# Kernel optimization log

Hardware: AMD Instinct MI355X
Metric: run time of the kernel (lower is better)

Reference implementation:

```python
import jax, jax.numpy as jnp
import numpy as np

N = 262144
D = 512
B = 1024  # number of segments/graphs (batch.max()+1 in the torch code)


def setup_inputs() -> dict:
    key = jax.random.key(0)
    k1, k2, k3, k4 = jax.random.split(key, 4)
    x = jax.random.normal(k1, (N, D), dtype=jnp.float32)
    batch = jnp.sort(jax.random.randint(k2, (N,), 0, B, dtype=jnp.int64))
    # score MLP params: Linear(D, D//4) -> Tanh -> Linear(D//4, 1)
    W1 = jax.random.normal(k3, (D, D // 4), dtype=jnp.float32) * (1.0 / np.sqrt(D))
    b1 = jnp.zeros((D // 4,), dtype=jnp.float32)
    W2 = jax.random.normal(k4, (D // 4, 1), dtype=jnp.float32) * (1.0 / np.sqrt(D // 4))
    b2 = jnp.zeros((1,), dtype=jnp.float32)
    return {"x": x, "batch": batch, "W1": W1, "b1": b1, "W2": W2, "b2": b2}


def reference(x, batch, W1, b1, W2, b2):
    # score MLP (dropout inactive at inference)
    scores = jnp.tanh(x @ W1 + b1) @ W2 + b2              # [N, 1]
    scores = scores - jnp.max(scores)                      # global max-shift for stability
    exp_s = jnp.exp(scores)                                # [N, 1]
    denom = jax.ops.segment_sum(exp_s, batch, num_segments=B)  # [B, 1]
    weight = exp_s / (denom[batch] + 1e-8)                 # [N, 1] segment softmax
    out = jax.ops.segment_sum(weight * x, batch, num_segments=B)  # [B, D]
    return out
```

## Files before the change

kernel.cpp:

```cpp
#include <hip/hip_runtime.h>
#include <hip/hip_bf16.h>

typedef _Float16 half8 __attribute__((ext_vector_type(8)));
typedef _Float16 half4v __attribute__((ext_vector_type(4)));
typedef float f32x4 __attribute__((ext_vector_type(4)));

#define BM 128
#define BK 64
#define LDK (BK + 8)

__global__ void prep_w1t(const float* __restrict__ W1, _Float16* __restrict__ W1T) {
    int idx = blockIdx.x * 256 + threadIdx.x;
    int n = idx >> 9;
    int k = idx & 511;
    W1T[idx] = (_Float16)W1[k * 128 + n];
}

__global__ __launch_bounds__(256) void score_kernel(
        const float* __restrict__ x, const _Float16* __restrict__ W1T,
        const float* __restrict__ b1, const float* __restrict__ W2,
        const float* __restrict__ b2, float* __restrict__ scores) {
    __shared__ _Float16 As[BM][LDK];
    __shared__ _Float16 Bs[128][LDK];
    const int tid = threadIdx.x;
    const int wave = tid >> 6, lane = tid & 63;
    const int quad = lane >> 4, col = lane & 15;
    const long row0 = (long)blockIdx.x * BM;

    f32x4 acc[2][8] = {};

    for (int kc = 0; kc < 512; kc += BK) {
        #pragma unroll
        for (int it = 0; it < 8; ++it) {
            int idx = it * 256 + tid;
            int r = idx >> 4, c4 = idx & 15;
            float4 v = *(const float4*)&x[(row0 + r) * 512 + kc + c4 * 4];
            half4v h; h[0] = (_Float16)v.x; h[1] = (_Float16)v.y;
                      h[2] = (_Float16)v.z; h[3] = (_Float16)v.w;
            *(half4v*)&As[r][c4 * 4] = h;
        }
        #pragma unroll
        for (int it = 0; it < 4; ++it) {
            int idx = it * 256 + tid;
            int n = idx >> 3, c8 = idx & 7;
            *(half8*)&Bs[n][c8 * 8] = *(const half8*)&W1T[n * 512 + kc + c8 * 8];
        }
        __syncthreads();
        #pragma unroll
        for (int ks = 0; ks < BK; ks += 32) {
            half8 a[2], bf[8];
            #pragma unroll
            for (int mt = 0; mt < 2; ++mt)
                a[mt] = *(half8*)&As[wave * 32 + mt * 16 + col][ks + quad * 8];
            #pragma unroll
            for (int nt = 0; nt < 8; ++nt)
                bf[nt] = *(half8*)&Bs[nt * 16 + col][ks + quad * 8];
            #pragma unroll
            for (int mt = 0; mt < 2; ++mt)
                #pragma unroll
                for (int nt = 0; nt < 8; ++nt)
                    acc[mt][nt] = __builtin_amdgcn_mfma_f32_16x16x32_f16(
                        a[mt], bf[nt], acc[mt][nt], 0, 0, 0);
        }
        __syncthreads();
    }

    float b1v[8], w2v[8];
    #pragma unroll
    for (int nt = 0; nt < 8; ++nt) {
        b1v[nt] = b1[nt * 16 + col];
        w2v[nt] = W2[nt * 16 + col];
    }
    float bias2 = b2[0];
    #pragma unroll
    for (int mt = 0; mt < 2; ++mt) {
        #pragma unroll
        for (int r = 0; r < 4; ++r) {
            float p = 0.f;
            #pragma unroll
            for (int nt = 0; nt < 8; ++nt)
                p += tanhf(acc[mt][nt][r] + b1v[nt]) * w2v[nt];
            #pragma unroll
            for (int off = 1; off < 16; off <<= 1) p += __shfl_xor(p, off);
            if (col == 0)
                scores[row0 + wave * 32 + mt * 16 + quad * 4 + r] = p + bias2;
        }
    }
}

__global__ void max_part(const float* __restrict__ scores, float* __restrict__ partial, int n) {
    __shared__ float red[256];
    int tid = threadIdx.x;
    float m = -1e30f;
    for (long i = (long)blockIdx.x * 256 + tid; i < n; i += (long)gridDim.x * 256)
        m = fmaxf(m, scores[i]);
    red[tid] = m; __syncthreads();
    for (int s = 128; s > 0; s >>= 1) {
        if (tid < s) red[tid] = fmaxf(red[tid], red[tid + s]);
        __syncthreads();
    }
    if (tid == 0) partial[blockIdx.x] = red[0];
}

__global__ void finalize_max(const float* __restrict__ partial, float* __restrict__ gmax,
                             float* __restrict__ denom, int nseg) {
    __shared__ float red[256];
    int tid = threadIdx.x;
    red[tid] = partial[tid]; __syncthreads();
    for (int s = 128; s > 0; s >>= 1) {
        if (tid < s) red[tid] = fmaxf(red[tid], red[tid + s]);
        __syncthreads();
    }
    if (tid == 0) gmax[0] = red[0];
    for (int b = tid; b < nseg; b += 256) denom[b] = 0.f;
}

__global__ void exp_denom(float* __restrict__ scores, const int* __restrict__ batch,
                          const float* __restrict__ gmax, float* __restrict__ denom, int n) {
    const int lane = threadIdx.x & 63;
    const float gm = gmax[0];
    for (long i = (long)blockIdx.x * blockDim.x + threadIdx.x; i < n;
         i += (long)gridDim.x * blockDim.x) {
        int seg = batch[i];
        float e = __expf(scores[i] - gm);
        scores[i] = e;
        float v = e;
        #pragma unroll
        for (int off = 1; off < 64; off <<= 1) {
            float ov = __shfl_down(v, off);
            int   os = __shfl_down(seg, off);
            if (lane + off < 64 && os == seg) v += ov;
        }
        int pseg = __shfl_up(seg, 1);
        if (lane == 0 || pseg != seg) atomicAdd(&denom[seg], v);
    }
}

__global__ void seg_starts(const int* __restrict__ batch, int* __restrict__ starts,
                           int n, int nseg) {
    for (long i = (long)blockIdx.x * blockDim.x + threadIdx.x; i < n;
         i += (long)gridDim.x * blockDim.x) {
        int s = batch[i];
        int p = (i == 0) ? -1 : batch[i - 1];
        for (int b = p + 1; b <= s; ++b) starts[b] = (int)i;
        if (i == n - 1)
            for (int b = s + 1; b <= nseg; ++b) starts[b] = n;
    }
}

__global__ __launch_bounds__(256) void pool_kernel(
        const float* __restrict__ x, const float* __restrict__ exps,
        const float* __restrict__ denom, const int* __restrict__ starts,
        float* __restrict__ out) {
    __shared__ f32x4 red[128];
    const int b = blockIdx.x;
    const int s0 = starts[b], s1 = starts[b + 1];
    const float dinv = 1.f / (denom[b] + 1e-8f);
    const int team = threadIdx.x >> 7;
    const int tl   = threadIdx.x & 127;
    const int c = tl * 4;
    f32x4 acc = {0.f, 0.f, 0.f, 0.f};
    #pragma unroll 4
    for (int i = s0 + team; i < s1; i += 2) {
        float w = exps[i] * dinv;
        f32x4 xv = *(const f32x4*)&x[(long)i * 512 + c];
        acc += w * xv;
    }
    if (team) red[tl] = acc;
    __syncthreads();
    if (!team) {
        f32x4 o = red[tl];
        acc += o;
        *(f32x4*)&out[(long)b * 512 + c] = acc;
    }
}

extern "C" void kernel_launch(void* const* d_in, const int* in_sizes, int n_in,
                              void* d_out, int out_size, void* d_ws, size_t ws_size,
                              hipStream_t stream) {
    const float* x     = (const float*)d_in[0];
    const int*   batch = (const int*)d_in[1];
    const float* W1    = (const float*)d_in[2];
    const float* b1    = (const float*)d_in[3];
    const float* W2    = (const float*)d_in[4];
    const float* b2    = (const float*)d_in[5];
    float* out = (float*)d_out;

    const int N = in_sizes[1];
    const int D = 512;
    const int NSEG = out_size / D;

    _Float16* W1T   = (_Float16*)d_ws;
    float* scores   = (float*)((char*)d_ws + 131072);
    float* partial  = scores + N;
    float* gmax     = partial + 256;
    float* denom    = partial + 512;
    int*   starts   = (int*)(denom + NSEG);

    prep_w1t<<<256, 256, 0, stream>>>(W1, W1T);
    seg_starts<<<256, 256, 0, stream>>>(batch, starts, N, NSEG);
    score_kernel<<<N / BM, 256, 0, stream>>>(x, W1T, b1, W2, b2, scores);
    max_part<<<256, 256, 0, stream>>>(scores, partial, N);
    finalize_max<<<1, 256, 0, stream>>>(partial, gmax, denom, NSEG);
    exp_denom<<<256, 256, 0, stream>>>(scores, batch, gmax, denom, N);
    pool_kernel<<<NSEG, 256, 0, stream>>>(x, scores, denom, starts, out);
}
```

Before: 807.6 us.

## Fuse score MLP, exp and segment pooling into one kernel with atomics

Merges the score GEMM, exponentiation and weighted segment pooling into a single kernel. Each 128-row tile exponentiates its scores in shared memory, then re-reads its own x rows (likely still in cache) and atomically accumulates per-segment sums and denominators. A final pass divides by the denominator. This removes the second full pass over x from HBM, the stored scores array and several small kernels. In exchange it drops the global max shift, which risks overflow for large scores, adds many float atomics, and hardcodes the output and segment sizes.

```diff
diff --git a/kernel.cpp b/kernel.cpp
--- a/kernel.cpp
+++ b/kernel.cpp
@@ -1,5 +1,4 @@
 #include <hip/hip_runtime.h>
-#include <hip/hip_bf16.h>
 
 typedef _Float16 half8 __attribute__((ext_vector_type(8)));
 typedef _Float16 half4v __attribute__((ext_vector_type(4)));
@@ -16,16 +15,28 @@
     W1T[idx] = (_Float16)W1[k * 128 + n];
 }
 
-__global__ __launch_bounds__(256) void score_kernel(
+__global__ void zero_kernel(float* __restrict__ out, float* __restrict__ denom) {
+    int id = blockIdx.x * 256 + threadIdx.x;
+    f32x4 z = {0.f, 0.f, 0.f, 0.f};
+    if (id < 131072)           ((f32x4*)out)[id] = z;
+    else                       ((f32x4*)denom)[id - 131072] = z;
+}
+
+__global__ __launch_bounds__(256) void fused_kernel(
         const float* __restrict__ x, const _Float16* __restrict__ W1T,
         const float* __restrict__ b1, const float* __restrict__ W2,
-        const float* __restrict__ b2, float* __restrict__ scores) {
+        const float* __restrict__ b2, const int* __restrict__ batch,
+        float* __restrict__ outacc, float* __restrict__ denom) {
     __shared__ _Float16 As[BM][LDK];
     __shared__ _Float16 Bs[128][LDK];
+    __shared__ float se[BM];
+    __shared__ int   sb[BM];
     const int tid = threadIdx.x;
     const int wave = tid >> 6, lane = tid & 63;
     const int quad = lane >> 4, col = lane & 15;
     const long row0 = (long)blockIdx.x * BM;
+
+    if (tid < BM) sb[tid] = batch[row0 + tid];
 
     f32x4 acc[2][8] = {};
 
@@ -83,96 +94,45 @@
             #pragma unroll
             for (int off = 1; off < 16; off <<= 1) p += __shfl_xor(p, off);
             if (col == 0)
-                scores[row0 + wave * 32 + mt * 16 + quad * 4 + r] = p + bias2;
+                se[wave * 32 + mt * 16 + quad * 4 + r] = __expf(p + bias2);
         }
     }
+    __syncthreads();
+
+    const int team = tid >> 7, tl = tid & 127;
+    const int c = tl * 4;
+    f32x4 pacc = {0.f, 0.f, 0.f, 0.f};
+    float esum = 0.f;
+    int curseg = sb[team];
+    for (int r = team; r < BM; r += 2) {
+        int s = sb[r];
+        if (s != curseg) {
+            atomicAdd(&outacc[(long)curseg * 512 + c + 0], pacc[0]);
+            atomicAdd(&outacc[(long)curseg * 512 + c + 1], pacc[1]);
+            atomicAdd(&outacc[(long)curseg * 512 + c + 2], pacc[2]);
+            atomicAdd(&outacc[(long)curseg * 512 + c + 3], pacc[3]);
+            if (tl == 0) atomicAdd(&denom[curseg], esum);
+            pacc = (f32x4){0.f, 0.f, 0.f, 0.f}; esum = 0.f; curseg = s;
+        }
+        float e = se[r];
+        f32x4 xv = *(const f32x4*)&x[(row0 + r) * 512 + c];
+        pacc += e * xv;
+        esum += e;
+    }
+    atomicAdd(&outacc[(long)curseg * 512 + c + 0], pacc[0]);
+    atomicAdd(&outacc[(long)curseg * 512 + c + 1], pacc[1]);
+    atomicAdd(&outacc[(long)curseg * 512 + c + 2], pacc[2]);
+    atomicAdd(&outacc[(long)curseg * 512 + c + 3], pacc[3]);
+    if (tl == 0) atomicAdd(&denom[curseg], esum);
 }
 
-__global__ void max_part(const float* __restrict__ scores, float* __restrict__ partial, int n) {
-    __shared__ float red[256];
-    int tid = threadIdx.x;
-    float m = -1e30f;
-    for (long i = (long)blockIdx.x * 256 + tid; i < n; i += (long)gridDim.x * 256)
-        m = fmaxf(m, scores[i]);
-    red[tid] = m; __syncthreads();
-    for (int s = 128; s > 0; s >>= 1) {
-        if (tid < s) red[tid] = fmaxf(red[tid], red[tid + s]);
-        __syncthreads();
-    }
-    if (tid == 0) partial[blockIdx.x] = red[0];
-}
-
-__global__ void finalize_max(const float* __restrict__ partial, float* __restrict__ gmax,
-                             float* __restrict__ denom, int nseg) {
-    __shared__ float red[256];
-    int tid = threadIdx.x;
-    red[tid] = partial[tid]; __syncthreads();
-    for (int s = 128; s > 0; s >>= 1) {
-        if (tid < s) red[tid] = fmaxf(red[tid], red[tid + s]);
-        __syncthreads();
-    }
-    if (tid == 0) gmax[0] = red[0];
-    for (int b = tid; b < nseg; b += 256) denom[b] = 0.f;
-}
-
-__global__ void exp_denom(float* __restrict__ scores, const int* __restrict__ batch,
-                          const float* __restrict__ gmax, float* __restrict__ denom, int n) {
-    const int lane = threadIdx.x & 63;
-    const float gm = gmax[0];
-    for (long i = (long)blockIdx.x * blockDim.x + threadIdx.x; i < n;
-         i += (long)gridDim.x * blockDim.x) {
-        int seg = batch[i];
-        float e = __expf(scores[i] - gm);
-        scores[i] = e;
-        float v = e;
-        #pragma unroll
-        for (int off = 1; off < 64; off <<= 1) {
-            float ov = __shfl_down(v, off);
-            int   os = __shfl_down(seg, off);
-            if (lane + off < 64 && os == seg) v += ov;
-        }
-        int pseg = __shfl_up(seg, 1);
-        if (lane == 0 || pseg != seg) atomicAdd(&denom[seg], v);
-    }
-}
-
-__global__ void seg_starts(const int* __restrict__ batch, int* __restrict__ starts,
-                           int n, int nseg) {
-    for (long i = (long)blockIdx.x * blockDim.x + threadIdx.x; i < n;
-         i += (long)gridDim.x * blockDim.x) {
-        int s = batch[i];
-        int p = (i == 0) ? -1 : batch[i - 1];
-        for (int b = p + 1; b <= s; ++b) starts[b] = (int)i;
-        if (i == n - 1)
-            for (int b = s + 1; b <= nseg; ++b) starts[b] = n;
-    }
-}
-
-__global__ __launch_bounds__(256) void pool_kernel(
-        const float* __restrict__ x, const float* __restrict__ exps,
-        const float* __restrict__ denom, const int* __restrict__ starts,
-        float* __restrict__ out) {
-    __shared__ f32x4 red[128];
+__global__ void finalize(float* __restrict__ out, const float* __restrict__ denom) {
     const int b = blockIdx.x;
-    const int s0 = starts[b], s1 = starts[b + 1];
+    const int c = threadIdx.x * 4;
     const float dinv = 1.f / (denom[b] + 1e-8f);
-    const int team = threadIdx.x >> 7;
-    const int tl   = threadIdx.x & 127;
-    const int c = tl * 4;
-    f32x4 acc = {0.f, 0.f, 0.f, 0.f};
-    #pragma unroll 4
-    for (int i = s0 + team; i < s1; i += 2) {
-        float w = exps[i] * dinv;
-        f32x4 xv = *(const f32x4*)&x[(long)i * 512 + c];
-        acc += w * xv;
-    }
-    if (team) red[tl] = acc;
-    __syncthreads();
-    if (!team) {
-        f32x4 o = red[tl];
-        acc += o;
-        *(f32x4*)&out[(long)b * 512 + c] = acc;
-    }
+    f32x4 v = *(f32x4*)&out[(long)b * 512 + c];
+    v *= dinv;
+    *(f32x4*)&out[(long)b * 512 + c] = v;
 }
 
 extern "C" void kernel_launch(void* const* d_in, const int* in_sizes, int n_in,
@@ -187,21 +147,12 @@
     float* out = (float*)d_out;
 
     const int N = in_sizes[1];
-    const int D = 512;
-    const int NSEG = out_size / D;
 
-    _Float16* W1T   = (_Float16*)d_ws;
-    float* scores   = (float*)((char*)d_ws + 131072);
-    float* partial  = scores + N;
-    float* gmax     = partial + 256;
-    float* denom    = partial + 512;
-    int*   starts   = (int*)(denom + NSEG);
+    _Float16* W1T = (_Float16*)d_ws;
+    float*    denom = (float*)((char*)d_ws + 131072);
 
     prep_w1t<<<256, 256, 0, stream>>>(W1, W1T);
-    seg_starts<<<256, 256, 0, stream>>>(batch, starts, N, NSEG);
-    score_kernel<<<N / BM, 256, 0, stream>>>(x, W1T, b1, W2, b2, scores);
-    max_part<<<256, 256, 0, stream>>>(scores, partial, N);
-    finalize_max<<<1, 256, 0, stream>>>(partial, gmax, denom, NSEG);
-    exp_denom<<<256, 256, 0, stream>>>(scores, batch, gmax, denom, N);
-    pool_kernel<<<NSEG, 256, 0, stream>>>(x, scores, denom, starts, out);
+    zero_kernel<<<513, 256, 0, stream>>>(out, denom);
+    fused_kernel<<<N / BM, 256, 0, stream>>>(x, W1T, b1, W2, b2, batch, out, denom);
+    finalize<<<1024, 128, 0, stream>>>(out, denom);
 }
```

Measured after the change: 810.2 us. Within noise of the previous version (+0.3%).
